# Optimization experiments

Hardware: AMD Instinct MI355X
Metric: run time of the kernel (lower is better)

Reference implementation:

```python
import jax, jax.numpy as jnp
import numpy as np

N_MC = 32
DT = 0.1
HIDDEN = 64
PROSPECTIVE_STEPS = 3
# scan_steps=3 -> first 3 of the hard-coded velocities
VELOCITIES = np.array([[0.2, 0.0], [0.0, 0.2], [0.15, 0.15]], dtype=np.float32)


def linear_interp_1d(x, out_size):
    """F.interpolate(mode='linear', align_corners=False) on last axis. x: [..., N]."""
    n = x.shape[-1]
    scale = n / out_size
    pos = (jnp.arange(out_size, dtype=x.dtype) + 0.5) * scale - 0.5
    pos = jnp.clip(pos, 0.0, n - 1)
    lo = jnp.floor(pos).astype(jnp.int32)
    hi = jnp.minimum(lo + 1, n - 1)
    w = pos - lo.astype(x.dtype)
    return x[..., lo] * (1.0 - w) + x[..., hi] * w


def setup_inputs() -> dict:
    key = jax.random.key(0)
    ks = jax.random.split(key, 8)
    B = 16384
    image = jax.random.uniform(ks[0], (B, 28, 28), dtype=jnp.float32)
    s = 1.0 / np.sqrt(N_MC)
    W_ff = jax.random.normal(ks[1], (N_MC, N_MC), dtype=jnp.float32) * s
    W_fb = jax.random.normal(ks[2], (N_MC, N_MC), dtype=jnp.float32) * s
    W_vel = jax.random.normal(ks[3], (N_MC, 2), dtype=jnp.float32) * s
    Wc1 = jax.random.normal(ks[4], (HIDDEN, 4 * N_MC), dtype=jnp.float32) * (1.0 / np.sqrt(4 * N_MC))
    bc1 = jnp.zeros((HIDDEN,), dtype=jnp.float32)
    Wc2 = jax.random.normal(ks[5], (10, HIDDEN), dtype=jnp.float32) * (1.0 / np.sqrt(HIDDEN))
    bc2 = jnp.zeros((10,), dtype=jnp.float32)
    return {"image": image, "W_ff": W_ff, "W_fb": W_fb, "W_vel": W_vel,
            "Wc1": Wc1, "bc1": bc1, "Wc2": Wc2, "bc2": bc2}


def _column_features(image, W_ff, W_fb, W_vel):
    B = image.shape[0]
    flat = image.reshape(B, -1)                       # [B, 784]
    flat_t = jnp.swapaxes(image, 1, 2).reshape(B, -1)  # transpose(0,1) per image
    sensory = linear_interp_1d(flat, N_MC) * 80.0     # [B, n_mc]
    topdown = linear_interp_1d(flat_t, N_MC) * 40.0   # [B, n_mc]

    r6 = jnp.zeros_like(sensory)                      # reset_state per image
    y_fb = jax.nn.relu(topdown @ W_fb.T)              # top-down feedback drive
    for v in VELOCITIES:                              # fixed 3-step scan
        vel_in = W_vel @ jnp.asarray(v)               # [n_mc]
        for _ in range(PROSPECTIVE_STEPS):            # fixed 3 prospective steps
            pred = r6 @ W_fb.T                        # top-down prediction of sensory drive
            eps_pos = jax.nn.relu(sensory - pred)
            eps_neg = jax.nn.relu(pred - sensory)
            y_ff = jax.nn.relu((eps_pos - eps_neg) @ W_ff.T)
            r6 = r6 + DT * (-r6 + y_ff + y_fb + vel_in)  # leaky L6 integrator
    feature = jnp.concatenate([y_ff, y_fb, r6, eps_pos + eps_neg], axis=-1)  # [B, 4*n_mc]
    return feature


def reference(image, W_ff, W_fb, W_vel, Wc1, bc1, Wc2, bc2):
    feature = jax.lax.stop_gradient(_column_features(image, W_ff, W_fb, W_vel))
    h = jax.nn.gelu(feature @ Wc1.T + bc1, approximate=False)
    logits = h @ Wc2.T + bc2                          # [B, 10]
    return logits
```

## Files before the change

kernel.cpp:

```cpp
#include <hip/hip_runtime.h>
#include <math.h>

typedef _Float16 f16x8 __attribute__((ext_vector_type(8)));
typedef float    f32x4 __attribute__((ext_vector_type(4)));

#define SCRW 132
#define MLDW 33

typedef __attribute__((address_space(3))) void lds_void;
typedef const __attribute__((address_space(1))) void glb_void;

__device__ __forceinline__ f32x4 mfma16(f16x8 a, f16x8 b, f32x4 c) {
  return __builtin_amdgcn_mfma_f32_16x16x32_f16(a, b, c, 0, 0, 0);
}

__device__ __forceinline__ void pack8(const float* v, f16x8& hi, f16x8& lo) {
#pragma unroll
  for (int j = 0; j < 8; ++j) {
    _Float16 h = (_Float16)v[j];
    hi[j] = h;
    lo[j] = (_Float16)(v[j] - (float)h);
  }
}

__device__ __forceinline__ f16x8 bfrag8(const float* p) {
  const f32x4* q = (const f32x4*)p;
  f32x4 w0 = q[0], w1 = q[1];
  f16x8 b;
#pragma unroll
  for (int j = 0; j < 4; ++j) { b[j] = (_Float16)w0[j]; b[j + 4] = (_Float16)w1[j]; }
  return b;
}

__device__ __forceinline__ void splitP(const float* p, f16x8& hi, f16x8& lo) {
  const f32x4* q = (const f32x4*)p;
  f32x4 a0 = q[0], a1 = q[1];
#pragma unroll
  for (int j = 0; j < 4; ++j) {
    _Float16 h0 = (_Float16)a0[j], h1 = (_Float16)a1[j];
    hi[j] = h0; hi[j + 4] = h1;
    lo[j]     = (_Float16)(a0[j] - (float)h0);
    lo[j + 4] = (_Float16)(a1[j] - (float)h1);
  }
}

__device__ __forceinline__ void load_chunk(const float* gsrc, float* lbase, int l) {
#pragma unroll
  for (int i = 0; i < 12; ++i)
    __builtin_amdgcn_global_load_lds((glb_void*)(gsrc + i * 256 + l * 4),
                                     (lds_void*)(lbase + i * 256), 16, 0, 0);
  __builtin_amdgcn_global_load_lds((glb_void*)(gsrc + 3072 + l),
                                   (lds_void*)(lbase + 3072), 4, 0, 0);
}

__global__ __launch_bounds__(256) void mnist_fused(
    const float* __restrict__ img,  const float* __restrict__ Wff,
    const float* __restrict__ Wfb,  const float* __restrict__ Wvel,
    const float* __restrict__ Wc1,  const float* __restrict__ bc1,
    const float* __restrict__ Wc2,  const float* __restrict__ bc2,
    float* __restrict__ out) {
  __shared__ float img_lds[4][784 * 4];
  __shared__ float scr_all[4][16 * SCRW];

  const int tid = threadIdx.x;
  const int wv = tid >> 6, l = tid & 63;
  const int g = l >> 4, c = l & 15;
  float* scr  = scr_all[wv];
  float* Mlds = scr;
  float* ibuf = img_lds[wv];
  const int s0 = blockIdx.x * 64 + wv * 16;
  const f32x4 zero = {0.f, 0.f, 0.f, 0.f};

  f32x4 rff[4], rfb[4];
  rff[0] = *(const f32x4*)(Wff + c * 32 + g * 8);
  rff[1] = *(const f32x4*)(Wff + c * 32 + g * 8 + 4);
  rff[2] = *(const f32x4*)(Wff + (16 + c) * 32 + g * 8);
  rff[3] = *(const f32x4*)(Wff + (16 + c) * 32 + g * 8 + 4);
  rfb[0] = *(const f32x4*)(Wfb + c * 32 + g * 8);
  rfb[1] = *(const f32x4*)(Wfb + c * 32 + g * 8 + 4);
  rfb[2] = *(const f32x4*)(Wfb + (16 + c) * 32 + g * 8);
  rfb[3] = *(const f32x4*)(Wfb + (16 + c) * 32 + g * 8 + 4);
  float rT0[8], rT1[8];
#pragma unroll
  for (int j = 0; j < 8; ++j) {
    rT0[j] = Wfb[(g * 8 + j) * 32 + c];
    rT1[j] = Wfb[(g * 8 + j) * 32 + 16 + c];
  }
  float2 wv0[4], wv1[4];
#pragma unroll
  for (int e = 0; e < 4; ++e) {
    wv0[e] = ((const float2*)Wvel)[g * 4 + e];
    wv1[e] = ((const float2*)Wvel)[16 + g * 4 + e];
  }
  __builtin_amdgcn_sched_barrier(0);

  load_chunk(img + (size_t)s0 * 784, ibuf, l);

  int loB[8], taB[8], tbB[8], loQ[8];
  float wB[8], wQ[8];
#pragma unroll
  for (int j = 0; j < 8; ++j) {
    int u = g * 8 + j;
    float pos = 24.5f * (float)u + 11.75f;
    loB[j] = (int)pos; wB[j] = pos - (float)loB[j];
    int lt = loB[j];
    taB[j] = (lt % 28) * 28 + lt / 28;
    lt += 1;
    tbB[j] = (lt % 28) * 28 + lt / 28;
  }
#pragma unroll
  for (int e2 = 0; e2 < 8; ++e2) {
    int u = (e2 >> 2) * 16 + g * 4 + (e2 & 3);
    float pos = 24.5f * (float)u + 11.75f;
    loQ[e2] = (int)pos; wQ[e2] = pos - (float)loQ[e2];
  }

  f16x8 bffh0, bffl0, bffh1, bffl1, bfbh0, bfbl0, bfbh1, bfbl1;
  {
    float t[8];
#pragma unroll
    for (int j = 0; j < 4; ++j) { t[j] = rff[0][j]; t[4 + j] = rff[1][j]; }
    pack8(t, bffh0, bffl0);
#pragma unroll
    for (int j = 0; j < 4; ++j) { t[j] = rff[2][j]; t[4 + j] = rff[3][j]; }
    pack8(t, bffh1, bffl1);
#pragma unroll
    for (int j = 0; j < 4; ++j) { t[j] = rfb[0][j]; t[4 + j] = rfb[1][j]; }
    pack8(t, bfbh0, bfbl0);
#pragma unroll
    for (int j = 0; j < 4; ++j) { t[j] = rfb[2][j]; t[4 + j] = rfb[3][j]; }
    pack8(t, bfbh1, bfbl1);
  }
  f16x8 aT0h, aT0l, aT1h, aT1l;
  pack8(rT0, aT0h, aT0l);
  pack8(rT1, aT1h, aT1l);

  f32x4 m00 = mfma16(aT0h, bffl0, mfma16(aT0l, bffh0, mfma16(aT0h, bffh0, zero)));
  f32x4 m01 = mfma16(aT0h, bffl1, mfma16(aT0l, bffh1, mfma16(aT0h, bffh1, zero)));
  f32x4 m10 = mfma16(aT1h, bffl0, mfma16(aT1l, bffh0, mfma16(aT1h, bffh0, zero)));
  f32x4 m11 = mfma16(aT1h, bffl1, mfma16(aT1l, bffh1, mfma16(aT1h, bffh1, zero)));
#pragma unroll
  for (int r = 0; r < 4; ++r) {
    Mlds[(g * 4 + r) * MLDW + c]            = m00[r];
    Mlds[(g * 4 + r) * MLDW + 16 + c]       = m01[r];
    Mlds[(16 + g * 4 + r) * MLDW + c]       = m10[r];
    Mlds[(16 + g * 4 + r) * MLDW + 16 + c]  = m11[r];
  }
  f16x8 nMt0h, nMt0l, nMt1h, nMt1l;
  {
    float m[8];
#pragma unroll
    for (int j = 0; j < 8; ++j) m[j] = -Mlds[(g * 8 + j) * MLDW + c];
    pack8(m, nMt0h, nMt0l);
#pragma unroll
    for (int j = 0; j < 8; ++j) m[j] = -Mlds[(g * 8 + j) * MLDW + 16 + c];
    pack8(m, nMt1h, nMt1l);
  }

  float sB[8] = {}, tB[8] = {}, sQ[8] = {};
#pragma unroll
  for (int ch = 0; ch < 4; ++ch) {
    asm volatile("s_waitcnt vmcnt(0)" ::: "memory");
    __builtin_amdgcn_sched_barrier(0);
    if ((c >> 2) == ch) {
      const float* base = ibuf + (c & 3) * 784;
#pragma unroll
      for (int j = 0; j < 8; ++j) {
        float a = base[loB[j]], b2 = base[loB[j] + 1];
        sB[j] = (a + (b2 - a) * wB[j]) * 80.0f;
      }
#pragma unroll
      for (int j = 0; j < 8; ++j) {
        float a = base[taB[j]], b2 = base[tbB[j]];
        tB[j] = (a + (b2 - a) * wB[j]) * 40.0f;
      }
#pragma unroll
      for (int e2 = 0; e2 < 8; ++e2) {
        float a = base[loQ[e2]], b2 = base[loQ[e2] + 1];
        sQ[e2] = (a + (b2 - a) * wQ[e2]) * 80.0f;
      }
    }
    if (ch < 3) load_chunk(img + (size_t)(s0 + (ch + 1) * 4) * 784, ibuf, l);
  }

  f16x8 snh, snl, tdh, tdl;
  pack8(sB, snh, snl);
  pack8(tB, tdh, tdl);
  f32x4 SN0 = {sQ[0], sQ[1], sQ[2], sQ[3]};
  f32x4 SN1 = {sQ[4], sQ[5], sQ[6], sQ[7]};

  f32x4 SF0 = mfma16(bffh0, snh, zero);
  SF0 += mfma16(bffl0, snh, mfma16(bffh0, snl, zero));
  f32x4 SF1 = mfma16(bffh1, snh, zero);
  SF1 += mfma16(bffl1, snh, mfma16(bffh1, snl, zero));
  f32x4 YFB0 = mfma16(bfbh0, tdh, zero);
  YFB0 += mfma16(bfbl0, tdh, mfma16(bfbh0, tdl, zero));
  f32x4 YFB1 = mfma16(bfbh1, tdh, zero);
  YFB1 += mfma16(bfbl1, tdh, mfma16(bfbh1, tdl, zero));
#pragma unroll
  for (int e = 0; e < 4; ++e) {
    YFB0[e] = fmaxf(YFB0[e], 0.f);
    YFB1[e] = fmaxf(YFB1[e], 0.f);
  }

  const int addrA = ((2 * (g & 1)) * 16 + c) * 4;
  const int addrB = addrA + 64;
  const bool hiG = (g >= 2);
  f32x4 r6q0 = zero, r6q1 = zero;
  f32x4 yf0 = zero, yf1 = zero, dq0 = zero, dq1 = zero;
  const float VX[3] = {0.2f, 0.0f, 0.15f};
  const float VY[3] = {0.0f, 0.2f, 0.15f};
#pragma unroll
  for (int v = 0; v < 3; ++v) {
    f32x4 vq0, vq1;
#pragma unroll
    for (int e = 0; e < 4; ++e) {
      vq0[e] = wv0[e].x * VX[v] + wv0[e].y * VY[v];
      vq1[e] = wv1[e].x * VX[v] + wv1[e].y * VY[v];
    }
#pragma unroll
    for (int st = 0; st < 3; ++st) {
      float t[8];
#pragma unroll
      for (int e = 0; e < 4; ++e) {
        int q0i = __float_as_int(r6q0[e]), q1i = __float_as_int(r6q1[e]);
        float a0 = __int_as_float(__builtin_amdgcn_ds_bpermute(addrA, q0i));
        float a1 = __int_as_float(__builtin_amdgcn_ds_bpermute(addrA, q1i));
        float b0 = __int_as_float(__builtin_amdgcn_ds_bpermute(addrB, q0i));
        float b1 = __int_as_float(__builtin_amdgcn_ds_bpermute(addrB, q1i));
        t[e]     = hiG ? a1 : a0;
        t[4 + e] = hiG ? b1 : b0;
      }
      f16x8 bh, bl;
      pack8(t, bh, bl);
      f32x4 y0 = mfma16(nMt0h, bh, SF0);
      y0 += mfma16(nMt0l, bh, mfma16(nMt0h, bl, zero));
      f32x4 y1 = mfma16(nMt1h, bh, SF1);
      y1 += mfma16(nMt1l, bh, mfma16(nMt1h, bl, zero));
      if (v == 2 && st == 2) {
        f32x4 p0 = mfma16(bfbh0, bh, zero);
        p0 += mfma16(bfbl0, bh, mfma16(bfbh0, bl, zero));
        f32x4 p1 = mfma16(bfbh1, bh, zero);
        p1 += mfma16(bfbl1, bh, mfma16(bfbh1, bl, zero));
#pragma unroll
        for (int e = 0; e < 4; ++e) { dq0[e] = SN0[e] - p0[e]; dq1[e] = SN1[e] - p1[e]; }
      }
#pragma unroll
      for (int e = 0; e < 4; ++e) {
        yf0[e] = fmaxf(y0[e], 0.f);
        yf1[e] = fmaxf(y1[e], 0.f);
        r6q0[e] += 0.1f * (yf0[e] - r6q0[e] + YFB0[e] + vq0[e]);
        r6q1[e] += 0.1f * (yf1[e] - r6q1[e] + YFB1[e] + vq1[e]);
      }
    }
  }

  {
    const int b0 = c * SCRW;
#pragma unroll
    for (int e = 0; e < 4; ++e) {
      scr[b0 +       g * 4 + e] = yf0[e];
      scr[b0 + 16  + g * 4 + e] = yf1[e];
      scr[b0 + 32  + g * 4 + e] = YFB0[e];
      scr[b0 + 48  + g * 4 + e] = YFB1[e];
      scr[b0 + 64  + g * 4 + e] = r6q0[e];
      scr[b0 + 80  + g * 4 + e] = r6q1[e];
      scr[b0 + 96  + g * 4 + e] = fabsf(dq0[e]);
      scr[b0 + 112 + g * 4 + e] = fabsf(dq1[e]);
    }
  }

  f32x4 acc0 = zero, acc1 = zero, acc2 = zero, acc3 = zero;
#pragma unroll
  for (int kb = 0; kb < 4; ++kb) {
    f16x8 fhi, flo;
    splitP(scr + c * SCRW + kb * 32 + g * 8, fhi, flo);
    const int ko = kb * 32 + g * 8;
    f16x8 b0 = bfrag8(Wc1 + (size_t)(c)      * 128 + ko);
    f16x8 b1 = bfrag8(Wc1 + (size_t)(16 + c) * 128 + ko);
    f16x8 b2 = bfrag8(Wc1 + (size_t)(32 + c) * 128 + ko);
    f16x8 b3 = bfrag8(Wc1 + (size_t)(48 + c) * 128 + ko);
    acc0 = mfma16(flo, b0, mfma16(fhi, b0, acc0));
    acc1 = mfma16(flo, b1, mfma16(fhi, b1, acc1));
    acc2 = mfma16(flo, b2, mfma16(fhi, b2, acc2));
    acc3 = mfma16(flo, b3, mfma16(fhi, b3, acc3));
  }
  float h[4][4];
  const float B0 = bc1[c], B1 = bc1[16 + c], B2 = bc1[32 + c], B3 = bc1[48 + c];
#pragma unroll
  for (int r = 0; r < 4; ++r) {
    float x0 = acc0[r] + B0, x1 = acc1[r] + B1, x2 = acc2[r] + B2, x3 = acc3[r] + B3;
    h[r][0] = 0.5f * x0 * (1.0f + erff(x0 * 0.70710678118654752f));
    h[r][1] = 0.5f * x1 * (1.0f + erff(x1 * 0.70710678118654752f));
    h[r][2] = 0.5f * x2 * (1.0f + erff(x2 * 0.70710678118654752f));
    h[r][3] = 0.5f * x3 * (1.0f + erff(x3 * 0.70710678118654752f));
  }
#pragma unroll
  for (int r = 0; r < 4; ++r) {
    int row = (g * 4 + r) * SCRW;
#pragma unroll
    for (int nb = 0; nb < 4; ++nb) scr[row + nb * 16 + c] = h[r][nb];
  }
  f32x4 accL = zero;
#pragma unroll
  for (int kb = 0; kb < 2; ++kb) {
    f16x8 hhi, hlo;
    splitP(scr + c * SCRW + kb * 32 + g * 8, hhi, hlo);
    f16x8 b;
    if (c < 10) {
      b = bfrag8(Wc2 + (size_t)c * 64 + kb * 32 + g * 8);
    } else {
#pragma unroll
      for (int j = 0; j < 8; ++j) b[j] = (_Float16)0.f;
    }
    accL = mfma16(hlo, b, mfma16(hhi, b, accL));
  }
  if (c < 10) {
    const float bb = bc2[c];
#pragma unroll
    for (int r = 0; r < 4; ++r)
      out[(size_t)(s0 + g * 4 + r) * 10 + c] = accL[r] + bb;
  }
}

extern "C" void kernel_launch(void* const* d_in, const int* in_sizes, int n_in,
                              void* d_out, int out_size, void* d_ws, size_t ws_size,
                              hipStream_t stream) {
  const float* img  = (const float*)d_in[0];
  const float* Wff  = (const float*)d_in[1];
  const float* Wfb  = (const float*)d_in[2];
  const float* Wvel = (const float*)d_in[3];
  const float* Wc1  = (const float*)d_in[4];
  const float* bc1  = (const float*)d_in[5];
  const float* Wc2  = (const float*)d_in[6];
  const float* bc2  = (const float*)d_in[7];
  float* out = (float*)d_out;
  const int B = in_sizes[0] / 784;
  const int grid = B / 64;
  hipLaunchKernelGGL(mnist_fused, dim3(grid), dim3(256), 0, stream,
                     img, Wff, Wfb, Wvel, Wc1, bc1, Wc2, bc2, out);
}
```

Measured before the change: 25.27 us.

## Halve samples per wave, double-buffer image loads, and raise occupancy

Each wave now processes 8 images instead of 16, and the grid doubles to cover the same batch. Images arrive in two-image chunks through two LDS buffers, with partial vmcnt waits so the next chunk loads while the current one is interpolated. Smaller LDS footprint and launch_bounds(256,2) should let two blocks share a CU, hiding more memory latency. The cost is that half of each 16-wide MFMA tile is duplicated or wasted work, so per-sample compute roughly doubles.

```diff
diff --git a/kernel.cpp b/kernel.cpp
--- a/kernel.cpp
+++ b/kernel.cpp
@@ -44,31 +44,33 @@
   }
 }
 
-__device__ __forceinline__ void load_chunk(const float* gsrc, float* lbase, int l) {
-#pragma unroll
-  for (int i = 0; i < 12; ++i)
+__device__ __forceinline__ void load_chunk2(const float* gsrc, float* lbase, int l) {
+#pragma unroll
+  for (int i = 0; i < 6; ++i)
     __builtin_amdgcn_global_load_lds((glb_void*)(gsrc + i * 256 + l * 4),
                                      (lds_void*)(lbase + i * 256), 16, 0, 0);
-  __builtin_amdgcn_global_load_lds((glb_void*)(gsrc + 3072 + l),
-                                   (lds_void*)(lbase + 3072), 4, 0, 0);
-}
-
-__global__ __launch_bounds__(256) void mnist_fused(
+  if (l < 8)
+    __builtin_amdgcn_global_load_lds((glb_void*)(gsrc + 1536 + l * 4),
+                                     (lds_void*)(lbase + 1536), 16, 0, 0);
+}
+
+__global__ __launch_bounds__(256, 2) void mnist_fused(
     const float* __restrict__ img,  const float* __restrict__ Wff,
     const float* __restrict__ Wfb,  const float* __restrict__ Wvel,
     const float* __restrict__ Wc1,  const float* __restrict__ bc1,
     const float* __restrict__ Wc2,  const float* __restrict__ bc2,
     float* __restrict__ out) {
-  __shared__ float img_lds[4][784 * 4];
-  __shared__ float scr_all[4][16 * SCRW];
+  __shared__ float img_lds[4][2][1568];
+  __shared__ float scr_all[4][1104];
 
   const int tid = threadIdx.x;
   const int wv = tid >> 6, l = tid & 63;
   const int g = l >> 4, c = l & 15;
   float* scr  = scr_all[wv];
   float* Mlds = scr;
-  float* ibuf = img_lds[wv];
-  const int s0 = blockIdx.x * 64 + wv * 16;
+  float* buf0 = &img_lds[wv][0][0];
+  float* buf1 = &img_lds[wv][1][0];
+  const int s0 = (blockIdx.x * 4 + wv) * 8;
   const f32x4 zero = {0.f, 0.f, 0.f, 0.f};
 
   f32x4 rff[4], rfb[4];
@@ -94,7 +96,9 @@
   }
   __builtin_amdgcn_sched_barrier(0);
 
-  load_chunk(img + (size_t)s0 * 784, ibuf, l);
+  load_chunk2(img + (size_t)(s0)     * 784, buf0, l);
+  load_chunk2(img + (size_t)(s0 + 2) * 784, buf1, l);
+  __builtin_amdgcn_sched_barrier(0);
 
   int loB[8], taB[8], tbB[8], loQ[8];
   float wB[8], wQ[8];
@@ -156,32 +160,51 @@
     for (int j = 0; j < 8; ++j) m[j] = -Mlds[(g * 8 + j) * MLDW + 16 + c];
     pack8(m, nMt1h, nMt1l);
   }
+  __builtin_amdgcn_sched_barrier(0);
 
   float sB[8] = {}, tB[8] = {}, sQ[8] = {};
-#pragma unroll
-  for (int ch = 0; ch < 4; ++ch) {
-    asm volatile("s_waitcnt vmcnt(0)" ::: "memory");
-    __builtin_amdgcn_sched_barrier(0);
-    if ((c >> 2) == ch) {
-      const float* base = ibuf + (c & 3) * 784;
-#pragma unroll
-      for (int j = 0; j < 8; ++j) {
-        float a = base[loB[j]], b2 = base[loB[j] + 1];
-        sB[j] = (a + (b2 - a) * wB[j]) * 80.0f;
-      }
-#pragma unroll
-      for (int j = 0; j < 8; ++j) {
-        float a = base[taB[j]], b2 = base[tbB[j]];
-        tB[j] = (a + (b2 - a) * wB[j]) * 40.0f;
-      }
-#pragma unroll
-      for (int e2 = 0; e2 < 8; ++e2) {
-        float a = base[loQ[e2]], b2 = base[loQ[e2] + 1];
-        sQ[e2] = (a + (b2 - a) * wQ[e2]) * 80.0f;
-      }
-    }
-    if (ch < 3) load_chunk(img + (size_t)(s0 + (ch + 1) * 4) * 784, ibuf, l);
-  }
+
+#define EXTRACT(CH, BUF)                                                     \
+  if ((c >> 1) == (CH)) {                                                    \
+    const float* base = (BUF) + (c & 1) * 784;                               \
+    _Pragma("unroll") for (int j = 0; j < 8; ++j) {                          \
+      float a = base[loB[j]], b2 = base[loB[j] + 1];                         \
+      sB[j] = (a + (b2 - a) * wB[j]) * 80.0f;                                \
+    }                                                                        \
+    _Pragma("unroll") for (int j = 0; j < 8; ++j) {                          \
+      float a = base[taB[j]], b2 = base[tbB[j]];                             \
+      tB[j] = (a + (b2 - a) * wB[j]) * 40.0f;                                \
+    }                                                                        \
+    _Pragma("unroll") for (int e2 = 0; e2 < 8; ++e2) {                       \
+      float a = base[loQ[e2]], b2 = base[loQ[e2] + 1];                       \
+      sQ[e2] = (a + (b2 - a) * wQ[e2]) * 80.0f;                              \
+    }                                                                        \
+  }
+
+  asm volatile("s_waitcnt vmcnt(7)" ::: "memory");
+  __builtin_amdgcn_sched_barrier(0);
+  EXTRACT(0, buf0)
+  asm volatile("s_waitcnt lgkmcnt(0)" ::: "memory");
+  __builtin_amdgcn_sched_barrier(0);
+  load_chunk2(img + (size_t)(s0 + 4) * 784, buf0, l);
+  __builtin_amdgcn_sched_barrier(0);
+
+  asm volatile("s_waitcnt vmcnt(7)" ::: "memory");
+  __builtin_amdgcn_sched_barrier(0);
+  EXTRACT(1, buf1)
+  asm volatile("s_waitcnt lgkmcnt(0)" ::: "memory");
+  __builtin_amdgcn_sched_barrier(0);
+  load_chunk2(img + (size_t)(s0 + 6) * 784, buf1, l);
+  __builtin_amdgcn_sched_barrier(0);
+
+  asm volatile("s_waitcnt vmcnt(7)" ::: "memory");
+  __builtin_amdgcn_sched_barrier(0);
+  EXTRACT(2, buf0)
+
+  asm volatile("s_waitcnt vmcnt(0)" ::: "memory");
+  __builtin_amdgcn_sched_barrier(0);
+  EXTRACT(3, buf1)
+#undef EXTRACT
 
   f16x8 snh, snl, tdh, tdl;
   pack8(sB, snh, snl);
@@ -255,7 +278,7 @@
     }
   }
 
-  {
+  if (c < 8) {
     const int b0 = c * SCRW;
 #pragma unroll
     for (int e = 0; e < 4; ++e) {
@@ -274,7 +297,7 @@
 #pragma unroll
   for (int kb = 0; kb < 4; ++kb) {
     f16x8 fhi, flo;
-    splitP(scr + c * SCRW + kb * 32 + g * 8, fhi, flo);
+    splitP(scr + (c & 7) * SCRW + kb * 32 + g * 8, fhi, flo);
     const int ko = kb * 32 + g * 8;
     f16x8 b0 = bfrag8(Wc1 + (size_t)(c)      * 128 + ko);
     f16x8 b1 = bfrag8(Wc1 + (size_t)(16 + c) * 128 + ko);
@@ -295,17 +318,19 @@
     h[r][2] = 0.5f * x2 * (1.0f + erff(x2 * 0.70710678118654752f));
     h[r][3] = 0.5f * x3 * (1.0f + erff(x3 * 0.70710678118654752f));
   }
-#pragma unroll
-  for (int r = 0; r < 4; ++r) {
-    int row = (g * 4 + r) * SCRW;
-#pragma unroll
-    for (int nb = 0; nb < 4; ++nb) scr[row + nb * 16 + c] = h[r][nb];
+  if (g < 2) {
+#pragma unroll
+    for (int r = 0; r < 4; ++r) {
+      int row = (g * 4 + r) * SCRW;
+#pragma unroll
+      for (int nb = 0; nb < 4; ++nb) scr[row + nb * 16 + c] = h[r][nb];
+    }
   }
   f32x4 accL = zero;
 #pragma unroll
   for (int kb = 0; kb < 2; ++kb) {
     f16x8 hhi, hlo;
-    splitP(scr + c * SCRW + kb * 32 + g * 8, hhi, hlo);
+    splitP(scr + (c & 7) * SCRW + kb * 32 + g * 8, hhi, hlo);
     f16x8 b;
     if (c < 10) {
       b = bfrag8(Wc2 + (size_t)c * 64 + kb * 32 + g * 8);
@@ -315,7 +340,7 @@
     }
     accL = mfma16(hlo, b, mfma16(hhi, b, accL));
   }
-  if (c < 10) {
+  if (c < 10 && g < 2) {
     const float bb = bc2[c];
 #pragma unroll
     for (int r = 0; r < 4; ++r)
@@ -336,7 +361,7 @@
   const float* bc2  = (const float*)d_in[7];
   float* out = (float*)d_out;
   const int B = in_sizes[0] / 784;
-  const int grid = B / 64;
+  const int grid = B / 32;
   hipLaunchKernelGGL(mnist_fused, dim3(grid), dim3(256), 0, stream,
                      img, Wff, Wfb, Wvel, Wc1, bc1, Wc2, bc2, out);
 }
```

New measurement: 28.34 us. 12.1% more time.
